# Performance work log

Measured on AMD Instinct MI355X. Metric: run time of the kernel, lower is better.

The kernel has to match this reference:

```python
import jax, jax.numpy as jnp
import numpy as np


def _windowed_attn(q, k, v, window_size, num_heads):
    # q, k, v: [B, T, D] with T % window_size == 0
    B, T, D = q.shape
    hd = D // num_heads
    scale = 1.0 / np.sqrt(hd).astype(np.float32)
    nw = T // window_size
    # [B, nw, w, H, hd]
    qh = q.reshape(B, nw, window_size, num_heads, hd)
    kh = k.reshape(B, nw, window_size, num_heads, hd)
    vh = v.reshape(B, nw, window_size, num_heads, hd)
    # attention scores per window: [B, nw, H, w, w]
    attn = jnp.einsum('bnqhd,bnkhd->bnhqk', qh, kh) * scale
    attn = jax.nn.softmax(attn, axis=-1)
    out = jnp.einsum('bnhqk,bnkhd->bnqhd', attn, vh)
    return out.reshape(B, T, D)


def setup_inputs() -> dict:
    key = jax.random.key(0)
    ks = jax.random.split(key, 6)
    B, D = 8, 512
    T1, T2 = 4096, 2048
    return {
        'q1': jax.random.normal(ks[0], (B, T1, D), dtype=jnp.float32),
        'k1': jax.random.normal(ks[1], (B, T1, D), dtype=jnp.float32),
        'v1': jax.random.normal(ks[2], (B, T1, D), dtype=jnp.float32),
        'q2': jax.random.normal(ks[3], (B, T2, D), dtype=jnp.float32),
        'k2': jax.random.normal(ks[4], (B, T2, D), dtype=jnp.float32),
        'v2': jax.random.normal(ks[5], (B, T2, D), dtype=jnp.float32),
        'window_size': 128,
        'num_heads': 8,
    }


def reference(q1, k1, v1, q2, k2, v2, window_size, num_heads):
    out1 = _windowed_attn(q1, k1, v1, window_size, num_heads)
    out2 = _windowed_attn(q2, k2, v2, window_size, num_heads)
    return (out1, out2)
```

## Files before the change

kernel.cpp:

```cpp
#include <hip/hip_runtime.h>
#include <hip/hip_bf16.h>

typedef __attribute__((ext_vector_type(4))) float f32x4;
typedef __attribute__((ext_vector_type(16))) float f32x16;
typedef __attribute__((ext_vector_type(8))) short bf16x8;

#define NH 8
#define HD 64
#define WSZ 128
#define DM 512

typedef __attribute__((address_space(3))) void lds_t;
typedef const __attribute__((address_space(1))) void gbl_t;

__device__ __forceinline__ unsigned int pk2bf(float lo, float hi) {
    union { __hip_bfloat162 h; unsigned int u; } r;
    r.h = __float22bfloat162_rn(make_float2(lo, hi));
    return r.u;
}

__device__ __forceinline__ bf16x8 pack8(f32x4 a, f32x4 b) {
    union { unsigned int u[4]; bf16x8 v; } r;
    r.u[0] = pk2bf(a[0], a[1]);
    r.u[1] = pk2bf(a[2], a[3]);
    r.u[2] = pk2bf(b[0], b[1]);
    r.u[3] = pk2bf(b[2], b[3]);
    return r.v;
}

__global__ __launch_bounds__(256, 2) void wattn_kernel(
    const float* __restrict__ q1, const float* __restrict__ k1,
    const float* __restrict__ v1, float* __restrict__ o1, int nw1,
    const float* __restrict__ q2, const float* __restrict__ k2,
    const float* __restrict__ v2, float* __restrict__ o2, int nw2,
    int nblk1)
{
    __shared__ __align__(16) float Kl[128 * 64];
    __shared__ __align__(16) float Vl[128 * 64];

    const int t = threadIdx.x;
    const int lane = t & 63;
    const int wid = t >> 6;
    const int hi = lane >> 5;
    const int c = lane & 31;

    int bid = blockIdx.x;
    const float *q, *k, *v; float* o; int nw;
    if (bid < nblk1) { q = q1; k = k1; v = v1; o = o1; nw = nw1; }
    else { bid -= nblk1; q = q2; k = k2; v = v2; o = o2; nw = nw2; }

    const int h = bid & (NH - 1);
    const int w = (bid / NH) % nw;
    const int b = (bid / NH) / nw;

    const size_t row0 = ((size_t)b * nw + w) * WSZ;
    const float* Qp = q + row0 * DM + h * HD;
    const float* Kp = k + row0 * DM + h * HD;
    const float* Vp = v + row0 * DM + h * HD;
    float* Op = o + row0 * DM + h * HD;

    const int qbase = wid * 32;

#pragma unroll
    for (int ii = 0; ii < 8; ++ii) {
        const int idx = wid * 8 + ii;
        const int row = idx * 4 + (lane >> 4);
        const int gs = lane & 15;
        const float* gk = Kp + (size_t)row * DM + ((gs ^ (row & 15)) << 2);
        const float* gv = Vp + (size_t)row * DM + (gs << 2);
        __builtin_amdgcn_global_load_lds((gbl_t*)gk,
            (lds_t*)((char*)Kl + idx * 1024), 16, 0, 0);
        __builtin_amdgcn_global_load_lds((gbl_t*)gv,
            (lds_t*)((char*)Vl + idx * 1024), 16, 0, 0);
    }

    bf16x8 qf[4];
#pragma unroll
    for (int ks = 0; ks < 4; ++ks) {
        const float* src = Qp + (size_t)(qbase + c) * DM + ks * 16 + hi * 8;
        f32x4 a = *reinterpret_cast<const f32x4*>(src);
        f32x4 bq = *reinterpret_cast<const f32x4*>(src + 4);
        qf[ks] = pack8(a, bq);
    }

    __syncthreads();

    f32x16 acc[4] = {};
#pragma unroll
    for (int ks = 0; ks < 4; ++ks) {
#pragma unroll
        for (int mf = 0; mf < 4; ++mf) {
            const int row = mf * 32 + c;
            const int r15 = c & 15;
            const int g0 = ks * 4 + hi * 2;
            f32x4 a = *reinterpret_cast<const f32x4*>(&Kl[row * 64 + ((g0 ^ r15) << 2)]);
            f32x4 bq = *reinterpret_cast<const f32x4*>(&Kl[row * 64 + (((g0 + 1) ^ r15) << 2)]);
            const bf16x8 kf = pack8(a, bq);
            acc[mf] = __builtin_amdgcn_mfma_f32_32x32x16_bf16(kf, qf[ks], acc[mf], 0, 0, 0);
        }
    }

    const float CEXP = 0.125f * 1.4426950408889634f;
    float mxa = fmaxf(acc[0][0], acc[1][0]);
    float mxb = fmaxf(acc[2][0], acc[3][0]);
#pragma unroll
    for (int e = 1; e < 16; ++e) {
        mxa = fmaxf(mxa, fmaxf(acc[0][e], acc[1][e]));
        mxb = fmaxf(mxb, fmaxf(acc[2][e], acc[3][e]));
    }
    float mx = fmaxf(mxa, mxb);
    mx = fmaxf(mx, __shfl_xor(mx, 32));
    const float mxc = mx * CEXP;
    float s0 = 0.f, s1 = 0.f, s2 = 0.f, s3 = 0.f;
#pragma unroll
    for (int e = 0; e < 16; ++e) {
        float p0 = exp2f(acc[0][e] * CEXP - mxc);
        float p1 = exp2f(acc[1][e] * CEXP - mxc);
        float p2 = exp2f(acc[2][e] * CEXP - mxc);
        float p3 = exp2f(acc[3][e] * CEXP - mxc);
        acc[0][e] = p0; acc[1][e] = p1; acc[2][e] = p2; acc[3][e] = p3;
        s0 += p0; s1 += p1; s2 += p2; s3 += p3;
    }
    float sum = (s0 + s1) + (s2 + s3);
    sum += __shfl_xor(sum, 32);
    const float rinv = 1.0f / sum;

    f32x16 oacc[2] = {};
#pragma unroll
    for (int f = 0; f < 4; ++f) {
#pragma unroll
        for (int p = 0; p < 2; ++p) {
            const int kb2 = f * 2 + p;
            unsigned int U0 = pk2bf(acc[f][8 * p + 0], acc[f][8 * p + 1]);
            unsigned int U1 = pk2bf(acc[f][8 * p + 2], acc[f][8 * p + 3]);
            unsigned int U2 = pk2bf(acc[f][8 * p + 4], acc[f][8 * p + 5]);
            unsigned int U3 = pk2bf(acc[f][8 * p + 6], acc[f][8 * p + 7]);
            asm volatile("v_permlane32_swap_b32 %0, %1" : "+v"(U0), "+v"(U2));
            asm volatile("v_permlane32_swap_b32 %0, %1" : "+v"(U1), "+v"(U3));
            union { unsigned int u[4]; bf16x8 v; } A;
            A.u[0] = U0; A.u[1] = U1; A.u[2] = U2; A.u[3] = U3;
            const int k0 = kb2 * 16 + hi * 8;
#pragma unroll
            for (int nf = 0; nf < 2; ++nf) {
                const float* vb = &Vl[k0 * 64 + nf * 32 + c];
                union { unsigned int u[4]; bf16x8 v; } V8;
                V8.u[0] = pk2bf(vb[0 * 64], vb[1 * 64]);
                V8.u[1] = pk2bf(vb[2 * 64], vb[3 * 64]);
                V8.u[2] = pk2bf(vb[4 * 64], vb[5 * 64]);
                V8.u[3] = pk2bf(vb[6 * 64], vb[7 * 64]);
                oacc[nf] = __builtin_amdgcn_mfma_f32_32x32x16_bf16(A.v, V8.v, oacc[nf], 0, 0, 0);
            }
        }
    }

#pragma unroll
    for (int reg = 0; reg < 16; ++reg) {
        const int qr = (reg & 3) + 8 * (reg >> 2) + 4 * hi;
        const float rv = __shfl(rinv, qr);
#pragma unroll
        for (int nf = 0; nf < 2; ++nf) {
            Op[(size_t)(qbase + qr) * DM + nf * 32 + c] = oacc[nf][reg] * rv;
        }
    }
}

extern "C" void kernel_launch(void* const* d_in, const int* in_sizes, int n_in,
                              void* d_out, int out_size, void* d_ws, size_t ws_size,
                              hipStream_t stream) {
    const float* q1 = (const float*)d_in[0];
    const float* k1 = (const float*)d_in[1];
    const float* v1 = (const float*)d_in[2];
    const float* q2 = (const float*)d_in[3];
    const float* k2 = (const float*)d_in[4];
    const float* v2 = (const float*)d_in[5];

    const int B = 8;
    const int nw1 = in_sizes[0] / (B * DM * WSZ);
    const int nw2 = in_sizes[3] / (B * DM * WSZ);

    float* o1 = (float*)d_out;
    float* o2 = o1 + (size_t)in_sizes[0];

    const int nblk1 = B * nw1 * NH;
    const int nblk2 = B * nw2 * NH;

    wattn_kernel<<<dim3(nblk1 + nblk2), dim3(256), 0, stream>>>(
        q1, k1, v1, o1, nw1, q2, k2, v2, o2, nw2, nblk1);
}
```

Measured before the change: 88.51 us.

## Process two attention tiles per block with double-buffered K/V prefetch

Each block now handles two (window, head) tiles. The K/V loads for the second tile are issued into a second LDS buffer while the first tile is computed, so global-load latency overlaps with MFMA work. LDS use doubles to 128KB per block and launch bounds drop to one block per CU. The grid is halved, which lowers occupancy and latency hiding across blocks in exchange for explicit overlap within each block.

```diff
diff --git a/kernel.cpp b/kernel.cpp
--- a/kernel.cpp
+++ b/kernel.cpp
@@ -28,140 +28,165 @@
     return r.v;
 }
 
-__global__ __launch_bounds__(256, 2) void wattn_kernel(
+__global__ __launch_bounds__(256, 1) void wattn_kernel(
     const float* __restrict__ q1, const float* __restrict__ k1,
     const float* __restrict__ v1, float* __restrict__ o1, int nw1,
     const float* __restrict__ q2, const float* __restrict__ k2,
     const float* __restrict__ v2, float* __restrict__ o2, int nw2,
-    int nblk1)
+    int nt1)
 {
-    __shared__ __align__(16) float Kl[128 * 64];
-    __shared__ __align__(16) float Vl[128 * 64];
+    __shared__ __align__(16) float Kl[2][128 * 64];
+    __shared__ __align__(16) float Vl[2][128 * 64];
 
     const int t = threadIdx.x;
     const int lane = t & 63;
     const int wid = t >> 6;
     const int hi = lane >> 5;
     const int c = lane & 31;
-
-    int bid = blockIdx.x;
-    const float *q, *k, *v; float* o; int nw;
-    if (bid < nblk1) { q = q1; k = k1; v = v1; o = o1; nw = nw1; }
-    else { bid -= nblk1; q = q2; k = k2; v = v2; o = o2; nw = nw2; }
-
-    const int h = bid & (NH - 1);
-    const int w = (bid / NH) % nw;
-    const int b = (bid / NH) / nw;
-
-    const size_t row0 = ((size_t)b * nw + w) * WSZ;
-    const float* Qp = q + row0 * DM + h * HD;
-    const float* Kp = k + row0 * DM + h * HD;
-    const float* Vp = v + row0 * DM + h * HD;
-    float* Op = o + row0 * DM + h * HD;
-
     const int qbase = wid * 32;
 
-#pragma unroll
-    for (int ii = 0; ii < 8; ++ii) {
-        const int idx = wid * 8 + ii;
-        const int row = idx * 4 + (lane >> 4);
-        const int gs = lane & 15;
-        const float* gk = Kp + (size_t)row * DM + ((gs ^ (row & 15)) << 2);
-        const float* gv = Vp + (size_t)row * DM + (gs << 2);
-        __builtin_amdgcn_global_load_lds((gbl_t*)gk,
-            (lds_t*)((char*)Kl + idx * 1024), 16, 0, 0);
-        __builtin_amdgcn_global_load_lds((gbl_t*)gv,
-            (lds_t*)((char*)Vl + idx * 1024), 16, 0, 0);
-    }
-
-    bf16x8 qf[4];
-#pragma unroll
-    for (int ks = 0; ks < 4; ++ks) {
-        const float* src = Qp + (size_t)(qbase + c) * DM + ks * 16 + hi * 8;
-        f32x4 a = *reinterpret_cast<const f32x4*>(src);
-        f32x4 bq = *reinterpret_cast<const f32x4*>(src + 4);
-        qf[ks] = pack8(a, bq);
-    }
+    auto tile_ptrs = [&](int ti, const float*& Qp, const float*& Kp,
+                         const float*& Vp, float*& Op) {
+        const float *q, *k, *v; float* o; int nw; int x = ti;
+        if (x < nt1) { q = q1; k = k1; v = v1; o = o1; nw = nw1; }
+        else { x -= nt1; q = q2; k = k2; v = v2; o = o2; nw = nw2; }
+        const int h = x & (NH - 1);
+        const int w = (x >> 3) % nw;
+        const int b = (x >> 3) / nw;
+        const size_t row0 = ((size_t)b * nw + w) * WSZ;
+        Qp = q + row0 * DM + h * HD;
+        Kp = k + row0 * DM + h * HD;
+        Vp = v + row0 * DM + h * HD;
+        Op = o + row0 * DM + h * HD;
+    };
+
+    auto burst = [&](int buf, const float* Kp_, const float* Vp_) {
+#pragma unroll
+        for (int ii = 0; ii < 8; ++ii) {
+            const int idx = wid * 8 + ii;
+            const int row = idx * 4 + (lane >> 4);
+            const int gs = lane & 15;
+            __builtin_amdgcn_global_load_lds(
+                (gbl_t*)(Kp_ + (size_t)row * DM + ((gs ^ (row & 15)) << 2)),
+                (lds_t*)((char*)&Kl[buf][0] + idx * 1024), 16, 0, 0);
+            __builtin_amdgcn_global_load_lds(
+                (gbl_t*)(Vp_ + (size_t)row * DM + (gs << 2)),
+                (lds_t*)((char*)&Vl[buf][0] + idx * 1024), 16, 0, 0);
+        }
+    };
+
+    auto loadq = [&](const float* Qp_, bf16x8 (&qf)[4]) {
+#pragma unroll
+        for (int ks = 0; ks < 4; ++ks) {
+            const float* src = Qp_ + (size_t)(qbase + c) * DM + ks * 16 + hi * 8;
+            qf[ks] = pack8(*reinterpret_cast<const f32x4*>(src),
+                           *reinterpret_cast<const f32x4*>(src + 4));
+        }
+    };
+
+    const float CEXP = 0.125f * 1.4426950408889634f;
+
+    auto compute_tile = [&](const float* KB, const float* VB,
+                            bf16x8 (&qf)[4], float* OpS) {
+        f32x16 acc[4] = {};
+#pragma unroll
+        for (int ks = 0; ks < 4; ++ks) {
+#pragma unroll
+            for (int mf = 0; mf < 4; ++mf) {
+                const int row = mf * 32 + c;
+                const int r15 = c & 15;
+                const int g0 = ks * 4 + hi * 2;
+                f32x4 a = *reinterpret_cast<const f32x4*>(&KB[row * 64 + ((g0 ^ r15) << 2)]);
+                f32x4 bq = *reinterpret_cast<const f32x4*>(&KB[row * 64 + (((g0 + 1) ^ r15) << 2)]);
+                acc[mf] = __builtin_amdgcn_mfma_f32_32x32x16_bf16(pack8(a, bq), qf[ks], acc[mf], 0, 0, 0);
+            }
+        }
+
+        float mxa = fmaxf(acc[0][0], acc[1][0]);
+        float mxb = fmaxf(acc[2][0], acc[3][0]);
+#pragma unroll
+        for (int e = 1; e < 16; ++e) {
+            mxa = fmaxf(mxa, fmaxf(acc[0][e], acc[1][e]));
+            mxb = fmaxf(mxb, fmaxf(acc[2][e], acc[3][e]));
+        }
+        float mx = fmaxf(mxa, mxb);
+        mx = fmaxf(mx, __shfl_xor(mx, 32));
+        const float mxc = mx * CEXP;
+        float s0 = 0.f, s1 = 0.f, s2 = 0.f, s3 = 0.f;
+#pragma unroll
+        for (int e = 0; e < 16; ++e) {
+            float p0 = exp2f(acc[0][e] * CEXP - mxc);
+            float p1 = exp2f(acc[1][e] * CEXP - mxc);
+            float p2 = exp2f(acc[2][e] * CEXP - mxc);
+            float p3 = exp2f(acc[3][e] * CEXP - mxc);
+            acc[0][e] = p0; acc[1][e] = p1; acc[2][e] = p2; acc[3][e] = p3;
+            s0 += p0; s1 += p1; s2 += p2; s3 += p3;
+        }
+        float sum = (s0 + s1) + (s2 + s3);
+        sum += __shfl_xor(sum, 32);
+        const float rinv = 1.0f / sum;
+
+        f32x16 oacc[2] = {};
+#pragma unroll
+        for (int f = 0; f < 4; ++f) {
+#pragma unroll
+            for (int p = 0; p < 2; ++p) {
+                const int kb2 = f * 2 + p;
+                unsigned int U0 = pk2bf(acc[f][8 * p + 0], acc[f][8 * p + 1]);
+                unsigned int U1 = pk2bf(acc[f][8 * p + 2], acc[f][8 * p + 3]);
+                unsigned int U2 = pk2bf(acc[f][8 * p + 4], acc[f][8 * p + 5]);
+                unsigned int U3 = pk2bf(acc[f][8 * p + 6], acc[f][8 * p + 7]);
+                asm volatile("v_permlane32_swap_b32 %0, %1" : "+v"(U0), "+v"(U2));
+                asm volatile("v_permlane32_swap_b32 %0, %1" : "+v"(U1), "+v"(U3));
+                union { unsigned int u[4]; bf16x8 v; } A;
+                A.u[0] = U0; A.u[1] = U1; A.u[2] = U2; A.u[3] = U3;
+                const int k0 = kb2 * 16 + hi * 8;
+#pragma unroll
+                for (int nf = 0; nf < 2; ++nf) {
+                    const float* vb = &VB[k0 * 64 + nf * 32 + c];
+                    union { unsigned int u[4]; bf16x8 v; } V8;
+                    V8.u[0] = pk2bf(vb[0 * 64], vb[1 * 64]);
+                    V8.u[1] = pk2bf(vb[2 * 64], vb[3 * 64]);
+                    V8.u[2] = pk2bf(vb[4 * 64], vb[5 * 64]);
+                    V8.u[3] = pk2bf(vb[6 * 64], vb[7 * 64]);
+                    oacc[nf] = __builtin_amdgcn_mfma_f32_32x32x16_bf16(A.v, V8.v, oacc[nf], 0, 0, 0);
+                }
+            }
+        }
+
+#pragma unroll
+        for (int reg = 0; reg < 16; ++reg) {
+            const int qr = (reg & 3) + 8 * (reg >> 2) + 4 * hi;
+            const float rv = __shfl(rinv, qr);
+#pragma unroll
+            for (int nf = 0; nf < 2; ++nf) {
+                OpS[(size_t)(qbase + qr) * DM + nf * 32 + c] = oacc[nf][reg] * rv;
+            }
+        }
+    };
+
+    const int t0 = blockIdx.x * 2;
+    const float *Qp, *Kp, *Vp; float* Op;
+
+    tile_ptrs(t0, Qp, Kp, Vp, Op);
+    burst(0, Kp, Vp);
+    bf16x8 qf0[4];
+    loadq(Qp, qf0);
+    float* Op0 = Op;
+
+    tile_ptrs(t0 + 1, Qp, Kp, Vp, Op);
 
     __syncthreads();
 
-    f32x16 acc[4] = {};
-#pragma unroll
-    for (int ks = 0; ks < 4; ++ks) {
-#pragma unroll
-        for (int mf = 0; mf < 4; ++mf) {
-            const int row = mf * 32 + c;
-            const int r15 = c & 15;
-            const int g0 = ks * 4 + hi * 2;
-            f32x4 a = *reinterpret_cast<const f32x4*>(&Kl[row * 64 + ((g0 ^ r15) << 2)]);
-            f32x4 bq = *reinterpret_cast<const f32x4*>(&Kl[row * 64 + (((g0 + 1) ^ r15) << 2)]);
-            const bf16x8 kf = pack8(a, bq);
-            acc[mf] = __builtin_amdgcn_mfma_f32_32x32x16_bf16(kf, qf[ks], acc[mf], 0, 0, 0);
-        }
-    }
-
-    const float CEXP = 0.125f * 1.4426950408889634f;
-    float mxa = fmaxf(acc[0][0], acc[1][0]);
-    float mxb = fmaxf(acc[2][0], acc[3][0]);
-#pragma unroll
-    for (int e = 1; e < 16; ++e) {
-        mxa = fmaxf(mxa, fmaxf(acc[0][e], acc[1][e]));
-        mxb = fmaxf(mxb, fmaxf(acc[2][e], acc[3][e]));
-    }
-    float mx = fmaxf(mxa, mxb);
-    mx = fmaxf(mx, __shfl_xor(mx, 32));
-    const float mxc = mx * CEXP;
-    float s0 = 0.f, s1 = 0.f, s2 = 0.f, s3 = 0.f;
-#pragma unroll
-    for (int e = 0; e < 16; ++e) {
-        float p0 = exp2f(acc[0][e] * CEXP - mxc);
-        float p1 = exp2f(acc[1][e] * CEXP - mxc);
-        float p2 = exp2f(acc[2][e] * CEXP - mxc);
-        float p3 = exp2f(acc[3][e] * CEXP - mxc);
-        acc[0][e] = p0; acc[1][e] = p1; acc[2][e] = p2; acc[3][e] = p3;
-        s0 += p0; s1 += p1; s2 += p2; s3 += p3;
-    }
-    float sum = (s0 + s1) + (s2 + s3);
-    sum += __shfl_xor(sum, 32);
-    const float rinv = 1.0f / sum;
-
-    f32x16 oacc[2] = {};
-#pragma unroll
-    for (int f = 0; f < 4; ++f) {
-#pragma unroll
-        for (int p = 0; p < 2; ++p) {
-            const int kb2 = f * 2 + p;
-            unsigned int U0 = pk2bf(acc[f][8 * p + 0], acc[f][8 * p + 1]);
-            unsigned int U1 = pk2bf(acc[f][8 * p + 2], acc[f][8 * p + 3]);
-            unsigned int U2 = pk2bf(acc[f][8 * p + 4], acc[f][8 * p + 5]);
-            unsigned int U3 = pk2bf(acc[f][8 * p + 6], acc[f][8 * p + 7]);
-            asm volatile("v_permlane32_swap_b32 %0, %1" : "+v"(U0), "+v"(U2));
-            asm volatile("v_permlane32_swap_b32 %0, %1" : "+v"(U1), "+v"(U3));
-            union { unsigned int u[4]; bf16x8 v; } A;
-            A.u[0] = U0; A.u[1] = U1; A.u[2] = U2; A.u[3] = U3;
-            const int k0 = kb2 * 16 + hi * 8;
-#pragma unroll
-            for (int nf = 0; nf < 2; ++nf) {
-                const float* vb = &Vl[k0 * 64 + nf * 32 + c];
-                union { unsigned int u[4]; bf16x8 v; } V8;
-                V8.u[0] = pk2bf(vb[0 * 64], vb[1 * 64]);
-                V8.u[1] = pk2bf(vb[2 * 64], vb[3 * 64]);
-                V8.u[2] = pk2bf(vb[4 * 64], vb[5 * 64]);
-                V8.u[3] = pk2bf(vb[6 * 64], vb[7 * 64]);
-                oacc[nf] = __builtin_amdgcn_mfma_f32_32x32x16_bf16(A.v, V8.v, oacc[nf], 0, 0, 0);
-            }
-        }
-    }
-
-#pragma unroll
-    for (int reg = 0; reg < 16; ++reg) {
-        const int qr = (reg & 3) + 8 * (reg >> 2) + 4 * hi;
-        const float rv = __shfl(rinv, qr);
-#pragma unroll
-        for (int nf = 0; nf < 2; ++nf) {
-            Op[(size_t)(qbase + qr) * DM + nf * 32 + c] = oacc[nf][reg] * rv;
-        }
-    }
+    burst(1, Kp, Vp);
+    bf16x8 qf1[4];
+    loadq(Qp, qf1);
+
+    compute_tile(&Kl[0][0], &Vl[0][0], qf0, Op0);
+
+    __syncthreads();
+
+    compute_tile(&Kl[1][0], &Vl[1][0], qf1, Op);
 }
 
 extern "C" void kernel_launch(void* const* d_in, const int* in_sizes, int n_in,
@@ -181,9 +206,10 @@
     float* o1 = (float*)d_out;
     float* o2 = o1 + (size_t)in_sizes[0];
 
-    const int nblk1 = B * nw1 * NH;
-    const int nblk2 = B * nw2 * NH;
-
-    wattn_kernel<<<dim3(nblk1 + nblk2), dim3(256), 0, stream>>>(
-        q1, k1, v1, o1, nw1, q2, k2, v2, o2, nw2, nblk1);
-}
+    const int nt1 = B * nw1 * NH;
+    const int nt2 = B * nw2 * NH;
+    const int nblk = (nt1 + nt2) / 2;
+
+    wattn_kernel<<<dim3(nblk), dim3(256), 0, stream>>>(
+        q1, k1, v1, o1, nw1, q2, k2, v2, o2, nw2, nt1);
+}
```

Measured after the change: 121.0 us. 1.37x slower.
